# Optimization experiments

Hardware: AMD Instinct MI355X
Metric: run time of the kernel (lower is better)

The kernel has to match this reference:

```python
import jax, jax.numpy as jnp
import numpy as np

B, D, N, F, O = 4096, 256, 128, 128, 256


def setup_inputs() -> dict:
    key = jax.random.key(0)
    ks = jax.random.split(key, 6)
    return {
        "x": jax.random.normal(ks[0], (B, D), dtype=jnp.float32),
        "node_weight": jax.random.normal(ks[1], (N, D + F, F), dtype=jnp.float32),  # torch.randn init
        "node_bias": jax.random.normal(ks[2], (N, F), dtype=jnp.float32),
        "attention": jax.random.normal(ks[3], (N, N), dtype=jnp.float32),
        "out_w": jax.random.normal(ks[4], (F, O), dtype=jnp.float32) * 0.05,  # Linear weight (transposed conv.)
        "out_b": jax.random.normal(ks[5], (O,), dtype=jnp.float32) * 0.05,
        "num_iterations": 3,
    }


def reference(x, node_weight, node_bias, attention, out_w, out_b, num_iterations):
    # connections[i, j] = softmax over j of attention row i
    conn = jax.nn.softmax(attention, axis=1)  # [N, N]
    # Split per-node weight: first F rows act on aggregated states, last D rows on x.
    W_s = node_weight[:, :F, :]   # [N, F, F]
    W_x = node_weight[:, F:, :]   # [N, D, F]
    # x contribution is identical every iteration; precompute once.
    xW = jnp.einsum('bd,ndf->nbf', x, W_x) + node_bias[:, None, :]  # [N, B, F]

    states0 = jnp.zeros((N, B, F), dtype=x.dtype)

    def step(states, _):
        agg = jnp.einsum('ij,jbf->ibf', conn, states)            # attention-weighted aggregation
        new = jax.nn.relu(jnp.einsum('nbf,nfg->nbg', agg, W_s) + xW)
        return new, None

    states, _ = jax.lax.scan(step, states0, None, length=num_iterations)
    final_state = states.mean(axis=0)                            # [B, F]
    return final_state @ out_w + out_b                           # [B, O]
```

## Files before the change

kernel.cpp:

```cpp
#include <hip/hip_runtime.h>

#define DEV __device__ __forceinline__

typedef __attribute__((ext_vector_type(8))) short short8;
typedef __attribute__((ext_vector_type(4))) float floatx4;
typedef __attribute__((ext_vector_type(4))) unsigned short ushort4v;
typedef __attribute__((ext_vector_type(8))) unsigned short ushort8v;

#define Bz 4096
#define Dz 256
#define Nz 128
#define Fz 128
#define Oz 256

static constexpr size_t OFF_CONN = 0;
static constexpr size_t OFF_WT   = 65536;
static constexpr size_t SZ_WT    = (size_t)Nz * 128 * 384 * 2;
static constexpr size_t OFF_OWT  = OFF_WT + SZ_WT;
static constexpr size_t OFF_XB   = OFF_OWT + 65536;
static constexpr size_t OFF_FIN  = OFF_XB + (size_t)Bz * Dz * 2;
static constexpr size_t OFF_ST   = OFF_FIN + (size_t)Bz * Fz * 2;

DEV unsigned short f2bf(float x) {
    unsigned u = __float_as_uint(x);
    u = (u + 0x7FFFu + ((u >> 16) & 1u)) >> 16;
    return (unsigned short)u;
}
DEV float bf2f(unsigned short h) {
    return __uint_as_float(((unsigned)h) << 16);
}

typedef const __attribute__((address_space(1))) void cglobal_void;
typedef __attribute__((address_space(3))) void lds_void;

DEV void gld_lds16(const void* g, void* l) {
    __builtin_amdgcn_global_load_lds((cglobal_void*)g, (lds_void*)l, 16, 0, 0);
}

__global__ __launch_bounds__(64) void k_softmax(const float* __restrict__ att,
                                                unsigned short* __restrict__ conn) {
    int i = blockIdx.x, t = threadIdx.x;
    float a0 = att[i * 128 + t];
    float a1 = att[i * 128 + 64 + t];
    float m = fmaxf(a0, a1);
    for (int o = 32; o > 0; o >>= 1) m = fmaxf(m, __shfl_down(m, o));
    m = __shfl(m, 0);
    float e0 = __expf(a0 - m), e1 = __expf(a1 - m);
    float s = e0 + e1;
    for (int o = 32; o > 0; o >>= 1) s += __shfl_down(s, o);
    s = __shfl(s, 0);
    float inv = 1.f / s;
    conn[i * 128 + t] = f2bf(e0 * inv);
    conn[i * 128 + 64 + t] = f2bf(e1 * inv);
}

__global__ __launch_bounds__(256) void k_transpose(const float* __restrict__ src,
                                                   unsigned short* __restrict__ dst,
                                                   int R, int C, int tilesC,
                                                   long sBatch, long dBatch) {
    __shared__ float ld[32][36];
    int tiles = (R / 32) * tilesC;
    int batch = blockIdx.x / tiles;
    int rem = blockIdx.x % tiles;
    int rt = rem / tilesC, ct = rem % tilesC;
    int t = threadIdx.x;
    int kr = t >> 3, c4 = (t & 7) * 4;
    float4 v = *(const float4*)&src[(size_t)batch * sBatch + (size_t)(rt * 32 + kr) * C + ct * 32 + c4];
    ld[kr][c4 + 0] = v.x; ld[kr][c4 + 1] = v.y; ld[kr][c4 + 2] = v.z; ld[kr][c4 + 3] = v.w;
    __syncthreads();
    int cr = kr, k4 = c4;
    ushort4v o;
    o[0] = f2bf(ld[k4 + 0][cr]);
    o[1] = f2bf(ld[k4 + 1][cr]);
    o[2] = f2bf(ld[k4 + 2][cr]);
    o[3] = f2bf(ld[k4 + 3][cr]);
    *(ushort4v*)&dst[(size_t)batch * dBatch + (size_t)(ct * 32 + cr) * R + rt * 32 + k4] = o;
}

__global__ __launch_bounds__(256) void k_convert(const float* __restrict__ src,
                                                 unsigned short* __restrict__ dst) {
    size_t idx = ((size_t)blockIdx.x * 256 + threadIdx.x) * 4;
    float4 v = *(const float4*)&src[idx];
    ushort4v o;
    o[0] = f2bf(v.x); o[1] = f2bf(v.y); o[2] = f2bf(v.z); o[3] = f2bf(v.w);
    *(ushort4v*)&dst[idx] = o;
}

__global__ __launch_bounds__(256) void k2_agg(const unsigned short* __restrict__ conn,
                                              unsigned short* __restrict__ ST) {
    __shared__ unsigned short lA[128 * 136];
    __shared__ unsigned short lB[2][32 * 128];
    int b = blockIdx.x;
    int t = threadIdx.x, wid = t >> 6, lane = t & 63, q = lane >> 4, cc = lane & 15;
    int wm = (wid >> 1) << 6, wn = (wid & 1) << 6;

#pragma unroll
    for (int it = 0; it < 8; it++) {
        int g = it * 256 + t;
        int row = g >> 4, cg = g & 15;
        *(short8*)&lA[row * 136 + cg * 8] = *(const short8*)&conn[row * 128 + cg * 8];
    }
    floatx4 acc[4][4];
#pragma unroll
    for (int mt = 0; mt < 4; mt++)
#pragma unroll
        for (int nt = 0; nt < 4; nt++) acc[mt][nt] = (floatx4){0.f, 0.f, 0.f, 0.f};

    auto STG = [&](int bufi, int kt) {
#pragma unroll
        for (int it = 0; it < 2; it++) {
            int g = it * 256 + t;
            int j = g >> 4, fg = g & 15;
            int lofs = __builtin_amdgcn_readfirstlane((it * 256 + (wid << 6)) * 8);
            gld_lds16(ST + ((size_t)(kt * 32 + j) * Bz + b) * Fz + fg * 8, &lB[bufi][0] + lofs);
        }
    };
    STG(0, 0);
    STG(1, 1);

#pragma unroll
    for (int kt = 0; kt < 4; kt++) {
        int cur = kt & 1;
        if (kt < 3) asm volatile("s_waitcnt vmcnt(2) lgkmcnt(0)" ::: "memory");
        else        asm volatile("s_waitcnt vmcnt(0) lgkmcnt(0)" ::: "memory");
        __builtin_amdgcn_s_barrier();
        __builtin_amdgcn_sched_barrier(0);
        short8 af[4];
#pragma unroll
        for (int mt = 0; mt < 4; mt++)
            af[mt] = *(const short8*)&lA[(wm + mt * 16 + cc) * 136 + kt * 32 + q * 8];
        short8 bf[4];
#pragma unroll
        for (int nt = 0; nt < 4; nt++) {
            short8 v;
#pragma unroll
            for (int e = 0; e < 8; e++)
                v[e] = (short)lB[cur][(q * 8 + e) * 128 + wn + nt * 16 + cc];
            bf[nt] = v;
        }
#pragma unroll
        for (int mt = 0; mt < 4; mt++)
#pragma unroll
            for (int nt = 0; nt < 4; nt++)
                acc[mt][nt] = __builtin_amdgcn_mfma_f32_16x16x32_bf16(af[mt], bf[nt], acc[mt][nt], 0, 0, 0);
        __builtin_amdgcn_sched_barrier(0);
        __builtin_amdgcn_s_barrier();
        if (kt + 2 < 4) STG(cur, kt + 2);
    }

#pragma unroll
    for (int mt = 0; mt < 4; mt++)
#pragma unroll
        for (int nt = 0; nt < 4; nt++) {
            int f = wn + nt * 16 + cc;
#pragma unroll
            for (int r = 0; r < 4; r++) {
                int il = wm + mt * 16 + q * 4 + r;
                lA[il * 128 + (f ^ ((il & 7) << 3))] = f2bf(acc[mt][nt][r]);
            }
        }
    __syncthreads();
#pragma unroll
    for (int it = 0; it < 8; it++) {
        int idx = it * 256 + t;
        int il = idx >> 4, ch = idx & 15;
        int sch = ch ^ (il & 7);
        ushort8v v = *(const ushort8v*)&lA[il * 128 + sch * 8];
        *(ushort8v*)&ST[((size_t)il * Bz + b) * Fz + ch * 8] = v;
    }
}

template <int KT0>
__global__ __launch_bounds__(256) void k3_fused(unsigned short* __restrict__ ST,
                                                const unsigned short* __restrict__ XB,
                                                const unsigned short* __restrict__ WT,
                                                const float* __restrict__ nb) {
    __shared__ unsigned short lds[3][2][128 * 32];
    int n = blockIdx.x >> 5, bt = blockIdx.x & 31;
    int t = threadIdx.x, wid = t >> 6, lane = t & 63, q = lane >> 4, cc = lane & 15;
    int wm = (wid >> 1) << 6, wn = (wid & 1) << 6;

    const unsigned short* Sg = ST + ((size_t)n * Bz + bt * 128) * Fz;
    const unsigned short* Xg = XB + (size_t)bt * 128 * Dz;
    const unsigned short* Bg = WT + (size_t)n * 128 * 384;

    floatx4 acc[4][4];
#pragma unroll
    for (int mt = 0; mt < 4; mt++)
#pragma unroll
        for (int nt = 0; nt < 4; nt++) acc[mt][nt] = (floatx4){0.f, 0.f, 0.f, 0.f};

    auto STAGE = [&](int bufi, int kt) {
#pragma unroll
        for (int it = 0; it < 2; it++) {
            int g = it * 256 + t;
            int row = g >> 2, kg = g & 3;
            int lofs = __builtin_amdgcn_readfirstlane((it * 256 + (wid << 6)) * 8);
            if (kt < 4)
                gld_lds16(Sg + (size_t)row * Fz + kt * 32 + kg * 8, &lds[bufi][0][0] + lofs);
            else
                gld_lds16(Xg + (size_t)row * Dz + (kt - 4) * 32 + kg * 8, &lds[bufi][0][0] + lofs);
            gld_lds16(Bg + (size_t)row * 384 + kt * 32 + kg * 8, &lds[bufi][1][0] + lofs);
        }
    };
    STAGE(0, KT0);
    STAGE(1, KT0 + 1);
    STAGE(2, KT0 + 2);

#pragma unroll
    for (int kt = KT0; kt < 12; kt++) {
        int cur = (kt - KT0) % 3;
        if (kt < 10)      asm volatile("s_waitcnt vmcnt(8) lgkmcnt(0)" ::: "memory");
        else if (kt < 11) asm volatile("s_waitcnt vmcnt(4) lgkmcnt(0)" ::: "memory");
        else              asm volatile("s_waitcnt vmcnt(0) lgkmcnt(0)" ::: "memory");
        __builtin_amdgcn_s_barrier();
        __builtin_amdgcn_sched_barrier(0);
        short8 af[4], bfr[4];
#pragma unroll
        for (int mt = 0; mt < 4; mt++)
            af[mt] = *(const short8*)&lds[cur][0][(wm + mt * 16 + cc) * 32 + q * 8];
#pragma unroll
        for (int nt = 0; nt < 4; nt++)
            bfr[nt] = *(const short8*)&lds[cur][1][(wn + nt * 16 + cc) * 32 + q * 8];
#pragma unroll
        for (int mt = 0; mt < 4; mt++)
#pragma unroll
            for (int nt = 0; nt < 4; nt++)
                acc[mt][nt] = __builtin_amdgcn_mfma_f32_16x16x32_bf16(af[mt], bfr[nt], acc[mt][nt], 0, 0, 0);
        __builtin_amdgcn_sched_barrier(0);
        __builtin_amdgcn_s_barrier();
        if (kt + 3 < 12) STAGE(cur, kt + 3);
    }

    unsigned short* outT = &lds[0][0][0];
#pragma unroll
    for (int nt = 0; nt < 4; nt++) {
        int f = wn + nt * 16 + cc;
        float bias = nb[n * Fz + f];
#pragma unroll
        for (int mt = 0; mt < 4; mt++) {
#pragma unroll
            for (int r = 0; r < 4; r++) {
                int bl = wm + mt * 16 + q * 4 + r;
                float v = acc[mt][nt][r] + bias;
                outT[bl * 128 + (f ^ ((bl & 7) << 3))] = f2bf(v > 0.f ? v : 0.f);
            }
        }
    }
    __syncthreads();
    size_t base = ((size_t)n * Bz + (size_t)bt * 128) * Fz;
#pragma unroll
    for (int it = 0; it < 8; it++) {
        int idx = it * 256 + t;
        int bl = idx >> 4, ch = idx & 15;
        int sch = ch ^ (bl & 7);
        ushort8v v = *(const ushort8v*)&outT[bl * 128 + sch * 8];
        *(ushort8v*)&ST[base + (size_t)idx * 8] = v;
    }
}

__global__ __launch_bounds__(256) void k4_mean(const unsigned short* __restrict__ S,
                                               unsigned short* __restrict__ fin) {
    int t = threadIdx.x;
    size_t base = (size_t)blockIdx.x * 2048 + (size_t)t * 8;
    float a[8] = {0.f, 0.f, 0.f, 0.f, 0.f, 0.f, 0.f, 0.f};
    for (int n = 0; n < Nz; n++) {
        ushort8v v = *(const ushort8v*)&S[(size_t)n * Bz * Fz + base];
#pragma unroll
        for (int e = 0; e < 8; e++) a[e] += bf2f(v[e]);
    }
    ushort8v o;
#pragma unroll
    for (int e = 0; e < 8; e++) o[e] = f2bf(a[e] * (1.f / 128.f));
    *(ushort8v*)&fin[base] = o;
}

__global__ __launch_bounds__(256) void k5_out(const unsigned short* __restrict__ fin,
                                              const unsigned short* __restrict__ owt,
                                              const float* __restrict__ ob,
                                              float* __restrict__ out) {
    __shared__ unsigned short lA[128 * 32];
    __shared__ unsigned short lB[128 * 32];
    int bt = blockIdx.x >> 1, ct = blockIdx.x & 1;
    int t = threadIdx.x, wid = t >> 6, lane = t & 63, q = lane >> 4, cc = lane & 15;
    int wm = (wid >> 1) << 6, wn = (wid & 1) << 6;

    const unsigned short* Ag = fin + (size_t)bt * 128 * Fz;
    const unsigned short* Bg = owt + (size_t)ct * 128 * Fz;

    floatx4 acc[4][4];
#pragma unroll
    for (int mt = 0; mt < 4; mt++)
#pragma unroll
        for (int nt = 0; nt < 4; nt++) acc[mt][nt] = (floatx4){0.f, 0.f, 0.f, 0.f};

    for (int kt = 0; kt < 4; kt++) {
#pragma unroll
        for (int it = 0; it < 2; it++) {
            int g = it * 256 + t;
            int row = g >> 2, kg = g & 3;
            int lofs = __builtin_amdgcn_readfirstlane((it * 256 + (wid << 6)) * 8);
            gld_lds16(Ag + (size_t)row * Fz + kt * 32 + kg * 8, lA + lofs);
            gld_lds16(Bg + (size_t)row * Fz + kt * 32 + kg * 8, lB + lofs);
        }
        __syncthreads();
        short8 af[4], bfr[4];
#pragma unroll
        for (int mt = 0; mt < 4; mt++)
            af[mt] = *(const short8*)&lA[(wm + mt * 16 + cc) * 32 + q * 8];
#pragma unroll
        for (int nt = 0; nt < 4; nt++)
            bfr[nt] = *(const short8*)&lB[(wn + nt * 16 + cc) * 32 + q * 8];
#pragma unroll
        for (int mt = 0; mt < 4; mt++)
#pragma unroll
            for (int nt = 0; nt < 4; nt++)
                acc[mt][nt] = __builtin_amdgcn_mfma_f32_16x16x32_bf16(af[mt], bfr[nt], acc[mt][nt], 0, 0, 0);
        __syncthreads();
    }
#pragma unroll
    for (int nt = 0; nt < 4; nt++) {
        int o = ct * 128 + wn + nt * 16 + cc;
        float bias = ob[o];
#pragma unroll
        for (int mt = 0; mt < 4; mt++) {
#pragma unroll
            for (int r = 0; r < 4; r++) {
                int b = bt * 128 + wm + mt * 16 + q * 4 + r;
                out[(size_t)b * Oz + o] = acc[mt][nt][r] + bias;
            }
        }
    }
}

extern "C" void kernel_launch(void* const* d_in, const int* in_sizes, int n_in,
                              void* d_out, int out_size, void* d_ws, size_t ws_size,
                              hipStream_t stream) {
    const float* x = (const float*)d_in[0];
    const float* nw = (const float*)d_in[1];
    const float* nb = (const float*)d_in[2];
    const float* att = (const float*)d_in[3];
    const float* ow = (const float*)d_in[4];
    const float* ob = (const float*)d_in[5];
    char* ws = (char*)d_ws;
    unsigned short* CONN = (unsigned short*)(ws + OFF_CONN);
    unsigned short* WT = (unsigned short*)(ws + OFF_WT);
    unsigned short* OWT = (unsigned short*)(ws + OFF_OWT);
    unsigned short* XB = (unsigned short*)(ws + OFF_XB);
    unsigned short* FIN = (unsigned short*)(ws + OFF_FIN);
    unsigned short* ST = (unsigned short*)(ws + OFF_ST);
    float* out = (float*)d_out;

    k_softmax<<<Nz, 64, 0, stream>>>(att, CONN);
    k_transpose<<<Nz * 48, 256, 0, stream>>>(nw, WT, 384, 128, 4, (long)384 * 128, (long)128 * 384);
    k_transpose<<<32, 256, 0, stream>>>(ow, OWT, 128, 256, 8, 0, 0);
    k_convert<<<(Bz * Dz) / 1024, 256, 0, stream>>>(x, XB);

    k3_fused<4><<<Nz * 32, 256, 0, stream>>>(ST, XB, WT, nb);

    for (int it = 0; it < 2; it++) {
        k2_agg<<<Bz, 256, 0, stream>>>(CONN, ST);
        k3_fused<0><<<Nz * 32, 256, 0, stream>>>(ST, XB, WT, nb);
    }

    k4_mean<<<(Bz * Fz) / 2048, 256, 0, stream>>>(ST, FIN);
    k5_out<<<64, 256, 0, stream>>>(FIN, OWT, ob, out);
}
```

Measured before the change: 404.0 us.

## Drop k2 double-buffering, split k3 launches in halves, unroll mean loop

Replaces the double-buffered async LDS staging in the aggregation kernel with a single buffer loaded synchronously each k-step, which removes the overlap of loads with MFMA but halves that LDS buffer. The fused node kernel is launched as two half-grids over batch tiles instead of one grid, which changes block scheduling and L2 locality of weights. The mean kernel's node loop gets an unroll pragma to expose more loads in flight. Together these look like experiments trading pipelining for simplicity and a different launch shape.

New measurement: 443.6 us. 9.8% more time.

```diff
diff --git a/kernel.cpp b/kernel.cpp
--- a/kernel.cpp
+++ b/kernel.cpp
@@ -89,7 +89,7 @@
 __global__ __launch_bounds__(256) void k2_agg(const unsigned short* __restrict__ conn,
                                               unsigned short* __restrict__ ST) {
     __shared__ unsigned short lA[128 * 136];
-    __shared__ unsigned short lB[2][32 * 128];
+    __shared__ unsigned short lB[32 * 128];
     int b = blockIdx.x;
     int t = threadIdx.x, wid = t >> 6, lane = t & 63, q = lane >> 4, cc = lane & 15;
     int wm = (wid >> 1) << 6, wn = (wid & 1) << 6;
@@ -106,25 +106,15 @@
 #pragma unroll
         for (int nt = 0; nt < 4; nt++) acc[mt][nt] = (floatx4){0.f, 0.f, 0.f, 0.f};
 
-    auto STG = [&](int bufi, int kt) {
+    for (int kt = 0; kt < 4; kt++) {
 #pragma unroll
         for (int it = 0; it < 2; it++) {
             int g = it * 256 + t;
             int j = g >> 4, fg = g & 15;
             int lofs = __builtin_amdgcn_readfirstlane((it * 256 + (wid << 6)) * 8);
-            gld_lds16(ST + ((size_t)(kt * 32 + j) * Bz + b) * Fz + fg * 8, &lB[bufi][0] + lofs);
-        }
-    };
-    STG(0, 0);
-    STG(1, 1);
-
-#pragma unroll
-    for (int kt = 0; kt < 4; kt++) {
-        int cur = kt & 1;
-        if (kt < 3) asm volatile("s_waitcnt vmcnt(2) lgkmcnt(0)" ::: "memory");
-        else        asm volatile("s_waitcnt vmcnt(0) lgkmcnt(0)" ::: "memory");
-        __builtin_amdgcn_s_barrier();
-        __builtin_amdgcn_sched_barrier(0);
+            gld_lds16(ST + ((size_t)(kt * 32 + j) * Bz + b) * Fz + fg * 8, lB + lofs);
+        }
+        __syncthreads();
         short8 af[4];
 #pragma unroll
         for (int mt = 0; mt < 4; mt++)
@@ -135,7 +125,7 @@
             short8 v;
 #pragma unroll
             for (int e = 0; e < 8; e++)
-                v[e] = (short)lB[cur][(q * 8 + e) * 128 + wn + nt * 16 + cc];
+                v[e] = (short)lB[(q * 8 + e) * 128 + wn + nt * 16 + cc];
             bf[nt] = v;
         }
 #pragma unroll
@@ -143,9 +133,7 @@
 #pragma unroll
             for (int nt = 0; nt < 4; nt++)
                 acc[mt][nt] = __builtin_amdgcn_mfma_f32_16x16x32_bf16(af[mt], bf[nt], acc[mt][nt], 0, 0, 0);
-        __builtin_amdgcn_sched_barrier(0);
-        __builtin_amdgcn_s_barrier();
-        if (kt + 2 < 4) STG(cur, kt + 2);
+        __syncthreads();
     }
 
 #pragma unroll
@@ -174,9 +162,10 @@
 __global__ __launch_bounds__(256) void k3_fused(unsigned short* __restrict__ ST,
                                                 const unsigned short* __restrict__ XB,
                                                 const unsigned short* __restrict__ WT,
-                                                const float* __restrict__ nb) {
+                                                const float* __restrict__ nb,
+                                                int bt0) {
     __shared__ unsigned short lds[3][2][128 * 32];
-    int n = blockIdx.x >> 5, bt = blockIdx.x & 31;
+    int n = blockIdx.x >> 4, bt = bt0 + (blockIdx.x & 15);
     int t = threadIdx.x, wid = t >> 6, lane = t & 63, q = lane >> 4, cc = lane & 15;
     int wm = (wid >> 1) << 6, wn = (wid & 1) << 6;
 
@@ -264,6 +253,7 @@
     int t = threadIdx.x;
     size_t base = (size_t)blockIdx.x * 2048 + (size_t)t * 8;
     float a[8] = {0.f, 0.f, 0.f, 0.f, 0.f, 0.f, 0.f, 0.f};
+#pragma unroll 8
     for (int n = 0; n < Nz; n++) {
         ushort8v v = *(const ushort8v*)&S[(size_t)n * Bz * Fz + base];
 #pragma unroll
@@ -356,11 +346,13 @@
     k_transpose<<<32, 256, 0, stream>>>(ow, OWT, 128, 256, 8, 0, 0);
     k_convert<<<(Bz * Dz) / 1024, 256, 0, stream>>>(x, XB);
 
-    k3_fused<4><<<Nz * 32, 256, 0, stream>>>(ST, XB, WT, nb);
+    k3_fused<4><<<Nz * 16, 256, 0, stream>>>(ST, XB, WT, nb, 0);
+    k3_fused<4><<<Nz * 16, 256, 0, stream>>>(ST, XB, WT, nb, 16);
 
     for (int it = 0; it < 2; it++) {
         k2_agg<<<Bz, 256, 0, stream>>>(CONN, ST);
-        k3_fused<0><<<Nz * 32, 256, 0, stream>>>(ST, XB, WT, nb);
+        k3_fused<0><<<Nz * 16, 256, 0, stream>>>(ST, XB, WT, nb, 0);
+        k3_fused<0><<<Nz * 16, 256, 0, stream>>>(ST, XB, WT, nb, 16);
     }
 
     k4_mean<<<(Bz * Fz) / 2048, 256, 0, stream>>>(ST, FIN);
```
